# Kernel optimization log

Measured on AMD Instinct MI355X. Metric: run time of the kernel, lower is better.

## Reference

```python
import jax, jax.numpy as jnp
import numpy as np

SEP = 2            # sep_token_id
B, S, H = 8, 4096, 768
MAX_SENT = 64      # = labels.size(1) in the original
STD = 0.02         # initializer_range


def setup_inputs() -> dict:
    key = jax.random.key(0)
    ks = jax.random.split(key, 6)
    hidden = jax.random.normal(ks[0], (B, S, H), jnp.float32)
    ids = jax.random.randint(ks[1], (B, S), 5, 30000, dtype=jnp.int64)
    # plant a sep every 64 tokens -> 64 seps, 64 non-empty sentences per row
    ids = ids.at[:, 63::64].set(SEP)
    W1 = jax.random.normal(ks[2], (H, 4096), jnp.float32) * STD
    b1 = jnp.zeros((4096,), jnp.float32)
    W2 = jax.random.normal(ks[3], (4096, 256), jnp.float32) * STD
    b2 = jnp.zeros((256,), jnp.float32)
    W3 = jax.random.normal(ks[4], (256, 2), jnp.float32) * STD
    b3 = jnp.zeros((2,), jnp.float32)
    return dict(hidden=hidden, input_ids=ids, W1=W1, b1=b1, W2=W2, b2=b2, W3=W3, b3=b3)


def _pool_row(h, ids):
    # h: [S, H], ids: [S] -> per-sentence means [MAX_SENT, H]
    sep = (ids == SEP)
    sep_i = sep.astype(jnp.int32)
    # exclusive cumsum: segment id = number of seps strictly before position t
    seg = jnp.cumsum(sep_i) - sep_i
    pos = jnp.arange(S)
    first_sep = jnp.argmax(sep)
    n_sep = sep_i.sum()
    # original includes the FIRST sep in sentence 0 but excludes later seps,
    # and excludes the last token of the trailing (post-last-sep) segment
    weight = jnp.where(sep, pos == first_sep, True)
    weight = weight & ~((pos == S - 1) & (seg == n_sep) & (n_sep > 0))
    # truncate to max_sentences: overflow segments land in a dump bucket
    seg_c = jnp.minimum(seg, MAX_SENT)
    hw = jnp.where(weight[:, None], h, 0.0)
    sums = jax.ops.segment_sum(hw, seg_c, num_segments=MAX_SENT + 1)[:MAX_SENT]
    cnts = jax.ops.segment_sum(weight.astype(h.dtype), seg_c, num_segments=MAX_SENT + 1)[:MAX_SENT]
    # empty (padding) segments -> zeros, matching the original zero-padding
    return jnp.where(cnts[:, None] > 0, sums / jnp.maximum(cnts, 1.0)[:, None], 0.0)


def reference(hidden, input_ids, W1, b1, W2, b2, W3, b3):
    # [B, MAX_SENT, H] per-sentence mean representations
    sent = jax.vmap(_pool_row)(hidden, input_ids)
    # classifier head (dropout = identity in eval); GELU is exact (torch nn.GELU default)
    x = jax.nn.gelu(jnp.einsum('bmh,hf->bmf', sent, W1) + b1, approximate=False)
    x = jax.nn.gelu(jnp.einsum('bmf,fg->bmg', x, W2) + b2, approximate=False)
    logits = jnp.einsum('bmg,gc->bmc', x, W3) + b3  # [B, MAX_SENT, 2]
    return logits
```

## Files before the change

### kernel.cpp

```cpp
#include <hip/hip_runtime.h>
#include <hip/hip_bf16.h>

#define SEP_ID 2
#define S_LEN  4096
#define HID    768
#define MAXS   64

using short8  = __attribute__((ext_vector_type(8))) short;
using floatx4 = __attribute__((ext_vector_type(4))) float;

__global__ void bounds_kernel(const int* __restrict__ ids,
                              int* __restrict__ sent_start,
                              int* __restrict__ sent_cnt) {
    const int b = blockIdx.x;
    const int t = threadIdx.x;
    const int* row = ids + (size_t)b * S_LEN;

    __shared__ int cnts[256];
    __shared__ int offs[256];
    __shared__ int sep_pos[S_LEN];
    __shared__ int total;

    int local[16];
    int c = 0;
    const int base = t * 16;
    #pragma unroll
    for (int i = 0; i < 16; ++i) {
        if (row[base + i] == SEP_ID) local[c++] = base + i;
    }
    cnts[t] = c;
    __syncthreads();
    if (t == 0) {
        int s = 0;
        for (int i = 0; i < 256; ++i) { offs[i] = s; s += cnts[i]; }
        total = s;
    }
    __syncthreads();
    {
        int o = offs[t];
        for (int i = 0; i < c; ++i) sep_pos[o + i] = local[i];
    }
    __syncthreads();

    const int n_sep = total;
    if (t < MAXS) {
        const int m = t;
        int start = 0, cnt = 0;
        if (n_sep == 0) {
            if (m == 0) { start = 0; cnt = S_LEN; }
        } else if (m < n_sep) {
            if (m == 0) { start = 0; cnt = sep_pos[0] + 1; }
            else { start = sep_pos[m - 1] + 1; cnt = sep_pos[m] - sep_pos[m - 1] - 1; }
        } else if (m == n_sep) {
            start = sep_pos[n_sep - 1] + 1;
            cnt = (S_LEN - 1) - start;
            if (cnt < 0) cnt = 0;
        }
        sent_start[b * MAXS + m] = start;
        sent_cnt[b * MAXS + m]  = cnt;
    }
}

__global__ __launch_bounds__(192) void pool_kernel(const float* __restrict__ hidden,
                                                   const int* __restrict__ sent_start,
                                                   const int* __restrict__ sent_cnt,
                                                   __hip_bfloat16* __restrict__ sent) {
    const int blk = blockIdx.x;
    const int b = blk >> 6;
    const int t = threadIdx.x;
    const int start = sent_start[blk];
    const int cnt   = sent_cnt[blk];

    const float4* base = (const float4*)(hidden + ((size_t)b * S_LEN + start) * HID);
    float ax = 0.f, ay = 0.f, az = 0.f, aw = 0.f;
    int i = 0;
    for (; i + 4 <= cnt; i += 4) {
        float4 v0 = base[(size_t)(i + 0) * 192 + t];
        float4 v1 = base[(size_t)(i + 1) * 192 + t];
        float4 v2 = base[(size_t)(i + 2) * 192 + t];
        float4 v3 = base[(size_t)(i + 3) * 192 + t];
        ax += v0.x + v1.x + v2.x + v3.x;
        ay += v0.y + v1.y + v2.y + v3.y;
        az += v0.z + v1.z + v2.z + v3.z;
        aw += v0.w + v1.w + v2.w + v3.w;
    }
    for (; i < cnt; ++i) {
        float4 v = base[(size_t)i * 192 + t];
        ax += v.x; ay += v.y; az += v.z; aw += v.w;
    }
    const float inv = (cnt > 0) ? 1.0f / (float)cnt : 0.0f;
    __hip_bfloat16* o = sent + (size_t)blk * HID + t * 4;
    o[0] = __float2bfloat16(ax * inv);
    o[1] = __float2bfloat16(ay * inv);
    o[2] = __float2bfloat16(az * inv);
    o[3] = __float2bfloat16(aw * inv);
}

__global__ __launch_bounds__(256) void tconv_kernel(const float* __restrict__ W1,
                                                    const float* __restrict__ W2,
                                                    __hip_bfloat16* __restrict__ W1T,
                                                    __hip_bfloat16* __restrict__ W2T) {
    __shared__ float tile[32][33];
    int id = blockIdx.x;
    const float* in; __hip_bfloat16* out; int K, N, n0, k0;
    if (id < 3072) {
        in = W1; out = W1T; K = 768; N = 4096;
        n0 = (id & 127) * 32; k0 = (id >> 7) * 32;
    } else {
        id -= 3072;
        in = W2; out = W2T; K = 4096; N = 256;
        n0 = (id & 7) * 32; k0 = (id >> 3) * 32;
    }
    const int c = threadIdx.x & 31;
    const int r = threadIdx.x >> 5;
    #pragma unroll
    for (int i = 0; i < 32; i += 8)
        tile[r + i][c] = in[(size_t)(k0 + r + i) * N + n0 + c];
    __syncthreads();
    #pragma unroll
    for (int i = 0; i < 32; i += 8)
        out[(size_t)(n0 + r + i) * K + k0 + c] = __float2bfloat16(tile[c][r + i]);
}

__device__ __forceinline__ float gelu_exact(float x) {
    return 0.5f * x * (1.0f + erff(x * 0.70710678118654752f));
}

__global__ __launch_bounds__(256) void gemm1_kernel(const __hip_bfloat16* __restrict__ A,
                                                    const __hip_bfloat16* __restrict__ BT,
                                                    const float* __restrict__ bias,
                                                    __hip_bfloat16* __restrict__ out) {
    const int n0 = blockIdx.x * 128;
    const int m0 = blockIdx.y * 64;
    const int t = threadIdx.x;
    const int w = t >> 6, l = t & 63;
    const int wm = (w >> 1) * 32;
    const int wn = (w & 1) * 64;

    __shared__ __hip_bfloat16 Al[64][40];
    __shared__ __hip_bfloat16 Bl[128][40];

    floatx4 acc[2][4] = {};

    const int r  = t >> 2;
    const int ch = (t & 3) * 8;
    const __hip_bfloat16* Ag  = A  + (size_t)(m0 + r) * 768 + ch;
    const __hip_bfloat16* Bg0 = BT + (size_t)(n0 + r) * 768 + ch;
    const __hip_bfloat16* Bg1 = BT + (size_t)(n0 + 64 + r) * 768 + ch;

    const int lr = l & 15;
    const int kq = (l >> 4) * 8;

    for (int k0 = 0; k0 < 768; k0 += 32) {
        short8 av  = *(const short8*)(Ag  + k0);
        short8 bv0 = *(const short8*)(Bg0 + k0);
        short8 bv1 = *(const short8*)(Bg1 + k0);
        __syncthreads();
        *(short8*)(&Al[r][ch])      = av;
        *(short8*)(&Bl[r][ch])      = bv0;
        *(short8*)(&Bl[64 + r][ch]) = bv1;
        __syncthreads();

        short8 a0 = *(const short8*)(&Al[wm + lr][kq]);
        short8 a1 = *(const short8*)(&Al[wm + 16 + lr][kq]);
        #pragma unroll
        for (int j = 0; j < 4; ++j) {
            short8 bj = *(const short8*)(&Bl[wn + j * 16 + lr][kq]);
            acc[0][j] = __builtin_amdgcn_mfma_f32_16x16x32_bf16(a0, bj, acc[0][j], 0, 0, 0);
            acc[1][j] = __builtin_amdgcn_mfma_f32_16x16x32_bf16(a1, bj, acc[1][j], 0, 0, 0);
        }
    }

    #pragma unroll
    for (int i = 0; i < 2; ++i) {
        #pragma unroll
        for (int j = 0; j < 4; ++j) {
            const int col  = n0 + wn + j * 16 + lr;
            const int rowb = m0 + wm + i * 16 + (l >> 4) * 4;
            const float bv = bias[col];
            #pragma unroll
            for (int rg = 0; rg < 4; ++rg) {
                float x = acc[i][j][rg] + bv;
                out[(size_t)(rowb + rg) * 4096 + col] = __float2bfloat16(gelu_exact(x));
            }
        }
    }
}

__global__ __launch_bounds__(256) void gemm2_kernel(const __hip_bfloat16* __restrict__ A,
                                                    const __hip_bfloat16* __restrict__ BT,
                                                    float* __restrict__ part) {
    const int n0 = blockIdx.x * 64;
    const int m0 = blockIdx.y * 64;
    const int s  = blockIdx.z;
    const int kb = s * 512;
    const int t = threadIdx.x;
    const int w = t >> 6, l = t & 63;
    const int wm = (w >> 1) * 32;
    const int wn = (w & 1) * 32;

    __shared__ __hip_bfloat16 Al[64][40];
    __shared__ __hip_bfloat16 Bl[64][40];

    floatx4 acc[2][2] = {};

    const int r  = t >> 2;
    const int ch = (t & 3) * 8;
    const __hip_bfloat16* Ag = A  + (size_t)(m0 + r) * 4096 + kb + ch;
    const __hip_bfloat16* Bg = BT + (size_t)(n0 + r) * 4096 + kb + ch;

    const int lr = l & 15;
    const int kq = (l >> 4) * 8;

    for (int k0 = 0; k0 < 512; k0 += 32) {
        short8 av = *(const short8*)(Ag + k0);
        short8 bv = *(const short8*)(Bg + k0);
        __syncthreads();
        *(short8*)(&Al[r][ch]) = av;
        *(short8*)(&Bl[r][ch]) = bv;
        __syncthreads();

        short8 a0 = *(const short8*)(&Al[wm + lr][kq]);
        short8 a1 = *(const short8*)(&Al[wm + 16 + lr][kq]);
        short8 b0 = *(const short8*)(&Bl[wn + lr][kq]);
        short8 b1 = *(const short8*)(&Bl[wn + 16 + lr][kq]);

        acc[0][0] = __builtin_amdgcn_mfma_f32_16x16x32_bf16(a0, b0, acc[0][0], 0, 0, 0);
        acc[0][1] = __builtin_amdgcn_mfma_f32_16x16x32_bf16(a0, b1, acc[0][1], 0, 0, 0);
        acc[1][0] = __builtin_amdgcn_mfma_f32_16x16x32_bf16(a1, b0, acc[1][0], 0, 0, 0);
        acc[1][1] = __builtin_amdgcn_mfma_f32_16x16x32_bf16(a1, b1, acc[1][1], 0, 0, 0);
    }

    float* po = part + (size_t)s * 512 * 256;
    #pragma unroll
    for (int i = 0; i < 2; ++i) {
        #pragma unroll
        for (int j = 0; j < 2; ++j) {
            const int col  = n0 + wn + j * 16 + lr;
            const int rowb = m0 + wm + i * 16 + (l >> 4) * 4;
            #pragma unroll
            for (int rg = 0; rg < 4; ++rg)
                po[(size_t)(rowb + rg) * 256 + col] = acc[i][j][rg];
        }
    }
}

__global__ __launch_bounds__(256) void rh_kernel(const float* __restrict__ part,
                                                 const float* __restrict__ b2,
                                                 const float* __restrict__ W3,
                                                 const float* __restrict__ b3,
                                                 float* __restrict__ out) {
    const int row = blockIdx.x;
    const int c = threadIdx.x;
    const int w = c >> 6, l = c & 63;

    float s = 0.f;
    #pragma unroll
    for (int k = 0; k < 8; ++k)
        s += part[((size_t)k * 512 + row) * 256 + c];
    const float x = gelu_exact(s + b2[c]);
    float y0 = x * W3[c * 2 + 0];
    float y1 = x * W3[c * 2 + 1];
    #pragma unroll
    for (int off = 32; off; off >>= 1) {
        y0 += __shfl_down(y0, off);
        y1 += __shfl_down(y1, off);
    }
    __shared__ float r0[4], r1[4];
    if (l == 0) { r0[w] = y0; r1[w] = y1; }
    __syncthreads();
    if (c == 0) out[row * 2 + 0] = r0[0] + r0[1] + r0[2] + r0[3] + b3[0];
    if (c == 1) out[row * 2 + 1] = r1[0] + r1[1] + r1[2] + r1[3] + b3[1];
}

extern "C" void kernel_launch(void* const* d_in, const int* in_sizes, int n_in,
                              void* d_out, int out_size, void* d_ws, size_t ws_size,
                              hipStream_t stream) {
    const float* hidden = (const float*)d_in[0];
    const int*   ids    = (const int*)d_in[1];
    const float* W1     = (const float*)d_in[2];
    const float* b1     = (const float*)d_in[3];
    const float* W2     = (const float*)d_in[4];
    const float* b2     = (const float*)d_in[5];
    const float* W3     = (const float*)d_in[6];
    const float* b3     = (const float*)d_in[7];
    float* out = (float*)d_out;

    char* ws = (char*)d_ws;
    int* sent_start        = (int*)(ws + 0);
    int* sent_cnt          = (int*)(ws + 2048);
    __hip_bfloat16* sentb  = (__hip_bfloat16*)(ws + 4096);
    __hip_bfloat16* W1T    = (__hip_bfloat16*)(ws + 790528);
    __hip_bfloat16* W2T    = (__hip_bfloat16*)(ws + 7081984);
    __hip_bfloat16* x1     = (__hip_bfloat16*)(ws + 9179136);
    float* part            = (float*)(ws + 13373440);

    bounds_kernel<<<8, 256, 0, stream>>>(ids, sent_start, sent_cnt);
    pool_kernel<<<512, 192, 0, stream>>>(hidden, sent_start, sent_cnt, sentb);
    tconv_kernel<<<4096, 256, 0, stream>>>(W1, W2, W1T, W2T);
    gemm1_kernel<<<dim3(32, 8), 256, 0, stream>>>(sentb, W1T, b1, x1);
    gemm2_kernel<<<dim3(4, 8, 8), 256, 0, stream>>>(x1, W2T, part);
    rh_kernel<<<512, 256, 0, stream>>>(part, b2, W3, b3, out);
}
```

Before: 207.8 us.

## Fuse all stages into one cooperative persistent kernel with grid syncs

```diff
diff --git a/kernel.cpp b/kernel.cpp
--- a/kernel.cpp
+++ b/kernel.cpp
@@ -1,5 +1,8 @@
 #include <hip/hip_runtime.h>
 #include <hip/hip_bf16.h>
+#include <hip/hip_cooperative_groups.h>
+
+namespace cg = cooperative_groups;
 
 #define SEP_ID 2
 #define S_LEN  4096
@@ -9,296 +12,302 @@
 using short8  = __attribute__((ext_vector_type(8))) short;
 using floatx4 = __attribute__((ext_vector_type(4))) float;
 
-__global__ void bounds_kernel(const int* __restrict__ ids,
-                              int* __restrict__ sent_start,
-                              int* __restrict__ sent_cnt) {
-    const int b = blockIdx.x;
-    const int t = threadIdx.x;
-    const int* row = ids + (size_t)b * S_LEN;
-
-    __shared__ int cnts[256];
-    __shared__ int offs[256];
-    __shared__ int sep_pos[S_LEN];
-    __shared__ int total;
-
-    int local[16];
-    int c = 0;
-    const int base = t * 16;
-    #pragma unroll
-    for (int i = 0; i < 16; ++i) {
-        if (row[base + i] == SEP_ID) local[c++] = base + i;
-    }
-    cnts[t] = c;
-    __syncthreads();
-    if (t == 0) {
-        int s = 0;
-        for (int i = 0; i < 256; ++i) { offs[i] = s; s += cnts[i]; }
-        total = s;
-    }
-    __syncthreads();
-    {
-        int o = offs[t];
-        for (int i = 0; i < c; ++i) sep_pos[o + i] = local[i];
-    }
-    __syncthreads();
-
-    const int n_sep = total;
-    if (t < MAXS) {
-        const int m = t;
-        int start = 0, cnt = 0;
-        if (n_sep == 0) {
-            if (m == 0) { start = 0; cnt = S_LEN; }
-        } else if (m < n_sep) {
-            if (m == 0) { start = 0; cnt = sep_pos[0] + 1; }
-            else { start = sep_pos[m - 1] + 1; cnt = sep_pos[m] - sep_pos[m - 1] - 1; }
-        } else if (m == n_sep) {
-            start = sep_pos[n_sep - 1] + 1;
-            cnt = (S_LEN - 1) - start;
-            if (cnt < 0) cnt = 0;
-        }
-        sent_start[b * MAXS + m] = start;
-        sent_cnt[b * MAXS + m]  = cnt;
-    }
-}
-
-__global__ __launch_bounds__(192) void pool_kernel(const float* __restrict__ hidden,
-                                                   const int* __restrict__ sent_start,
-                                                   const int* __restrict__ sent_cnt,
-                                                   __hip_bfloat16* __restrict__ sent) {
-    const int blk = blockIdx.x;
-    const int b = blk >> 6;
-    const int t = threadIdx.x;
-    const int start = sent_start[blk];
-    const int cnt   = sent_cnt[blk];
-
-    const float4* base = (const float4*)(hidden + ((size_t)b * S_LEN + start) * HID);
-    float ax = 0.f, ay = 0.f, az = 0.f, aw = 0.f;
-    int i = 0;
-    for (; i + 4 <= cnt; i += 4) {
-        float4 v0 = base[(size_t)(i + 0) * 192 + t];
-        float4 v1 = base[(size_t)(i + 1) * 192 + t];
-        float4 v2 = base[(size_t)(i + 2) * 192 + t];
-        float4 v3 = base[(size_t)(i + 3) * 192 + t];
-        ax += v0.x + v1.x + v2.x + v3.x;
-        ay += v0.y + v1.y + v2.y + v3.y;
-        az += v0.z + v1.z + v2.z + v3.z;
-        aw += v0.w + v1.w + v2.w + v3.w;
-    }
-    for (; i < cnt; ++i) {
-        float4 v = base[(size_t)i * 192 + t];
-        ax += v.x; ay += v.y; az += v.z; aw += v.w;
-    }
-    const float inv = (cnt > 0) ? 1.0f / (float)cnt : 0.0f;
-    __hip_bfloat16* o = sent + (size_t)blk * HID + t * 4;
-    o[0] = __float2bfloat16(ax * inv);
-    o[1] = __float2bfloat16(ay * inv);
-    o[2] = __float2bfloat16(az * inv);
-    o[3] = __float2bfloat16(aw * inv);
-}
-
-__global__ __launch_bounds__(256) void tconv_kernel(const float* __restrict__ W1,
-                                                    const float* __restrict__ W2,
-                                                    __hip_bfloat16* __restrict__ W1T,
-                                                    __hip_bfloat16* __restrict__ W2T) {
-    __shared__ float tile[32][33];
-    int id = blockIdx.x;
-    const float* in; __hip_bfloat16* out; int K, N, n0, k0;
-    if (id < 3072) {
-        in = W1; out = W1T; K = 768; N = 4096;
-        n0 = (id & 127) * 32; k0 = (id >> 7) * 32;
-    } else {
-        id -= 3072;
-        in = W2; out = W2T; K = 4096; N = 256;
-        n0 = (id & 7) * 32; k0 = (id >> 3) * 32;
-    }
-    const int c = threadIdx.x & 31;
-    const int r = threadIdx.x >> 5;
-    #pragma unroll
-    for (int i = 0; i < 32; i += 8)
-        tile[r + i][c] = in[(size_t)(k0 + r + i) * N + n0 + c];
-    __syncthreads();
-    #pragma unroll
-    for (int i = 0; i < 32; i += 8)
-        out[(size_t)(n0 + r + i) * K + k0 + c] = __float2bfloat16(tile[c][r + i]);
-}
+struct Params {
+    const float* hidden; const int* ids;
+    const float* W1; const float* b1;
+    const float* W2; const float* b2;
+    const float* W3; const float* b3;
+    float* out;
+    int* sent_start; int* sent_cnt;
+    __hip_bfloat16* sentb; __hip_bfloat16* W1T; __hip_bfloat16* W2T;
+    __hip_bfloat16* x1; float* part;
+};
 
 __device__ __forceinline__ float gelu_exact(float x) {
     return 0.5f * x * (1.0f + erff(x * 0.70710678118654752f));
 }
 
-__global__ __launch_bounds__(256) void gemm1_kernel(const __hip_bfloat16* __restrict__ A,
-                                                    const __hip_bfloat16* __restrict__ BT,
-                                                    const float* __restrict__ bias,
-                                                    __hip_bfloat16* __restrict__ out) {
-    const int n0 = blockIdx.x * 128;
-    const int m0 = blockIdx.y * 64;
+__global__ __launch_bounds__(384) void mega_kernel(Params p) {
+    cg::grid_group grid = cg::this_grid();
+    const int blk = blockIdx.x;
     const int t = threadIdx.x;
-    const int w = t >> 6, l = t & 63;
-    const int wm = (w >> 1) * 32;
-    const int wn = (w & 1) * 64;
-
-    __shared__ __hip_bfloat16 Al[64][40];
-    __shared__ __hip_bfloat16 Bl[128][40];
-
-    floatx4 acc[2][4] = {};
-
-    const int r  = t >> 2;
-    const int ch = (t & 3) * 8;
-    const __hip_bfloat16* Ag  = A  + (size_t)(m0 + r) * 768 + ch;
-    const __hip_bfloat16* Bg0 = BT + (size_t)(n0 + r) * 768 + ch;
-    const __hip_bfloat16* Bg1 = BT + (size_t)(n0 + 64 + r) * 768 + ch;
-
-    const int lr = l & 15;
-    const int kq = (l >> 4) * 8;
-
-    for (int k0 = 0; k0 < 768; k0 += 32) {
-        short8 av  = *(const short8*)(Ag  + k0);
-        short8 bv0 = *(const short8*)(Bg0 + k0);
-        short8 bv1 = *(const short8*)(Bg1 + k0);
+
+    __shared__ __align__(16) char smem[18688];
+
+    if (blk < 8) {
+        int* cnts = (int*)smem;
+        int* offs = cnts + 256;
+        int* sep_pos = offs + 256;
+        int* totalp = sep_pos + 4096;
+        const int* row = p.ids + (size_t)blk * S_LEN;
+        int local[16]; int c = 0;
+        if (t < 256) {
+            const int base = t * 16;
+            #pragma unroll
+            for (int i = 0; i < 16; ++i)
+                if (row[base + i] == SEP_ID) local[c++] = base + i;
+            cnts[t] = c;
+        }
         __syncthreads();
-        *(short8*)(&Al[r][ch])      = av;
-        *(short8*)(&Bl[r][ch])      = bv0;
-        *(short8*)(&Bl[64 + r][ch]) = bv1;
+        if (t == 0) {
+            int s = 0;
+            for (int i = 0; i < 256; ++i) { offs[i] = s; s += cnts[i]; }
+            *totalp = s;
+        }
         __syncthreads();
-
-        short8 a0 = *(const short8*)(&Al[wm + lr][kq]);
-        short8 a1 = *(const short8*)(&Al[wm + 16 + lr][kq]);
-        #pragma unroll
-        for (int j = 0; j < 4; ++j) {
-            short8 bj = *(const short8*)(&Bl[wn + j * 16 + lr][kq]);
-            acc[0][j] = __builtin_amdgcn_mfma_f32_16x16x32_bf16(a0, bj, acc[0][j], 0, 0, 0);
-            acc[1][j] = __builtin_amdgcn_mfma_f32_16x16x32_bf16(a1, bj, acc[1][j], 0, 0, 0);
-        }
-    }
-
-    #pragma unroll
-    for (int i = 0; i < 2; ++i) {
-        #pragma unroll
-        for (int j = 0; j < 4; ++j) {
-            const int col  = n0 + wn + j * 16 + lr;
-            const int rowb = m0 + wm + i * 16 + (l >> 4) * 4;
-            const float bv = bias[col];
-            #pragma unroll
-            for (int rg = 0; rg < 4; ++rg) {
-                float x = acc[i][j][rg] + bv;
-                out[(size_t)(rowb + rg) * 4096 + col] = __float2bfloat16(gelu_exact(x));
-            }
-        }
-    }
-}
-
-__global__ __launch_bounds__(256) void gemm2_kernel(const __hip_bfloat16* __restrict__ A,
-                                                    const __hip_bfloat16* __restrict__ BT,
-                                                    float* __restrict__ part) {
-    const int n0 = blockIdx.x * 64;
-    const int m0 = blockIdx.y * 64;
-    const int s  = blockIdx.z;
-    const int kb = s * 512;
-    const int t = threadIdx.x;
-    const int w = t >> 6, l = t & 63;
-    const int wm = (w >> 1) * 32;
-    const int wn = (w & 1) * 32;
-
-    __shared__ __hip_bfloat16 Al[64][40];
-    __shared__ __hip_bfloat16 Bl[64][40];
-
-    floatx4 acc[2][2] = {};
-
-    const int r  = t >> 2;
-    const int ch = (t & 3) * 8;
-    const __hip_bfloat16* Ag = A  + (size_t)(m0 + r) * 4096 + kb + ch;
-    const __hip_bfloat16* Bg = BT + (size_t)(n0 + r) * 4096 + kb + ch;
-
-    const int lr = l & 15;
-    const int kq = (l >> 4) * 8;
-
-    for (int k0 = 0; k0 < 512; k0 += 32) {
-        short8 av = *(const short8*)(Ag + k0);
-        short8 bv = *(const short8*)(Bg + k0);
+        if (t < 256) { int o = offs[t]; for (int i = 0; i < c; ++i) sep_pos[o + i] = local[i]; }
         __syncthreads();
-        *(short8*)(&Al[r][ch]) = av;
-        *(short8*)(&Bl[r][ch]) = bv;
-        __syncthreads();
-
-        short8 a0 = *(const short8*)(&Al[wm + lr][kq]);
-        short8 a1 = *(const short8*)(&Al[wm + 16 + lr][kq]);
-        short8 b0 = *(const short8*)(&Bl[wn + lr][kq]);
-        short8 b1 = *(const short8*)(&Bl[wn + 16 + lr][kq]);
-
-        acc[0][0] = __builtin_amdgcn_mfma_f32_16x16x32_bf16(a0, b0, acc[0][0], 0, 0, 0);
-        acc[0][1] = __builtin_amdgcn_mfma_f32_16x16x32_bf16(a0, b1, acc[0][1], 0, 0, 0);
-        acc[1][0] = __builtin_amdgcn_mfma_f32_16x16x32_bf16(a1, b0, acc[1][0], 0, 0, 0);
-        acc[1][1] = __builtin_amdgcn_mfma_f32_16x16x32_bf16(a1, b1, acc[1][1], 0, 0, 0);
-    }
-
-    float* po = part + (size_t)s * 512 * 256;
-    #pragma unroll
-    for (int i = 0; i < 2; ++i) {
-        #pragma unroll
-        for (int j = 0; j < 2; ++j) {
-            const int col  = n0 + wn + j * 16 + lr;
-            const int rowb = m0 + wm + i * 16 + (l >> 4) * 4;
-            #pragma unroll
-            for (int rg = 0; rg < 4; ++rg)
-                po[(size_t)(rowb + rg) * 256 + col] = acc[i][j][rg];
-        }
-    }
-}
-
-__global__ __launch_bounds__(256) void rh_kernel(const float* __restrict__ part,
-                                                 const float* __restrict__ b2,
-                                                 const float* __restrict__ W3,
-                                                 const float* __restrict__ b3,
-                                                 float* __restrict__ out) {
-    const int row = blockIdx.x;
-    const int c = threadIdx.x;
-    const int w = c >> 6, l = c & 63;
-
-    float s = 0.f;
-    #pragma unroll
-    for (int k = 0; k < 8; ++k)
-        s += part[((size_t)k * 512 + row) * 256 + c];
-    const float x = gelu_exact(s + b2[c]);
-    float y0 = x * W3[c * 2 + 0];
-    float y1 = x * W3[c * 2 + 1];
-    #pragma unroll
-    for (int off = 32; off; off >>= 1) {
-        y0 += __shfl_down(y0, off);
-        y1 += __shfl_down(y1, off);
-    }
-    __shared__ float r0[4], r1[4];
-    if (l == 0) { r0[w] = y0; r1[w] = y1; }
-    __syncthreads();
-    if (c == 0) out[row * 2 + 0] = r0[0] + r0[1] + r0[2] + r0[3] + b3[0];
-    if (c == 1) out[row * 2 + 1] = r1[0] + r1[1] + r1[2] + r1[3] + b3[1];
+        const int n_sep = *totalp;
+        if (t < MAXS) {
+            const int m = t;
+            int start = 0, cnt = 0;
+            if (n_sep == 0) {
+                if (m == 0) { start = 0; cnt = S_LEN; }
+            } else if (m < n_sep) {
+                if (m == 0) { start = 0; cnt = sep_pos[0] + 1; }
+                else { start = sep_pos[m - 1] + 1; cnt = sep_pos[m] - sep_pos[m - 1] - 1; }
+            } else if (m == n_sep) {
+                start = sep_pos[n_sep - 1] + 1;
+                cnt = (S_LEN - 1) - start;
+                if (cnt < 0) cnt = 0;
+            }
+            p.sent_start[blk * MAXS + m] = start;
+            p.sent_cnt[blk * MAXS + m]  = cnt;
+        }
+    } else {
+        float* tile = (float*)smem;
+        const int c = t & 31;
+        const int r = t >> 5;
+        for (int id0 = blk - 8; id0 < 4096; id0 += 248) {
+            const float* in; __hip_bfloat16* outw; int K, N, n0, k0;
+            if (id0 < 3072) { in = p.W1; outw = p.W1T; K = 768;  N = 4096;
+                              n0 = (id0 & 127) * 32; k0 = (id0 >> 7) * 32; }
+            else { const int id = id0 - 3072;
+                   in = p.W2; outw = p.W2T; K = 4096; N = 256;
+                   n0 = (id & 7) * 32; k0 = (id >> 3) * 32; }
+            if (t < 256) {
+                #pragma unroll
+                for (int i = 0; i < 32; i += 8)
+                    tile[(r + i) * 33 + c] = in[(size_t)(k0 + r + i) * N + n0 + c];
+            }
+            __syncthreads();
+            if (t < 256) {
+                #pragma unroll
+                for (int i = 0; i < 32; i += 8)
+                    outw[(size_t)(n0 + r + i) * K + k0 + c] = __float2bfloat16(tile[c * 33 + r + i]);
+            }
+            __syncthreads();
+        }
+    }
+
+    grid.sync();
+
+    {
+        const int which = t / 192;
+        const int u = t - which * 192;
+        const int sidx = blk * 2 + which;
+        const int b = sidx >> 6;
+        const int start = p.sent_start[sidx];
+        const int cnt   = p.sent_cnt[sidx];
+        const float4* base = (const float4*)(p.hidden + ((size_t)b * S_LEN + start) * HID);
+        float ax = 0.f, ay = 0.f, az = 0.f, aw = 0.f;
+        int i = 0;
+        for (; i + 8 <= cnt; i += 8) {
+            float4 v[8];
+            #pragma unroll
+            for (int j = 0; j < 8; ++j) v[j] = base[(size_t)(i + j) * 192 + u];
+            #pragma unroll
+            for (int j = 0; j < 8; ++j) { ax += v[j].x; ay += v[j].y; az += v[j].z; aw += v[j].w; }
+        }
+        for (; i < cnt; ++i) {
+            float4 v = base[(size_t)i * 192 + u];
+            ax += v.x; ay += v.y; az += v.z; aw += v.w;
+        }
+        const float inv = (cnt > 0) ? 1.0f / (float)cnt : 0.0f;
+        __hip_bfloat16* o = p.sentb + (size_t)sidx * HID + u * 4;
+        o[0] = __float2bfloat16(ax * inv);
+        o[1] = __float2bfloat16(ay * inv);
+        o[2] = __float2bfloat16(az * inv);
+        o[3] = __float2bfloat16(aw * inv);
+    }
+
+    grid.sync();
+
+    {
+        const int n0 = (blk & 31) * 128;
+        const int m0 = (blk >> 5) * 64;
+        const int w = t >> 6, l = t & 63;
+        const int wm = (w >> 1) * 32;
+        const int wn = (w & 1) * 64;
+        __hip_bfloat16* Al = (__hip_bfloat16*)smem;
+        __hip_bfloat16* Bl = Al + 64 * 40;
+        floatx4 acc[2][4] = {};
+        const int r  = t >> 2;
+        const int ch = (t & 3) * 8;
+        const __hip_bfloat16 *Ag = nullptr, *Bg0 = nullptr, *Bg1 = nullptr;
+        if (t < 256) {
+            Ag  = p.sentb + (size_t)(m0 + r) * 768 + ch;
+            Bg0 = p.W1T + (size_t)(n0 + r) * 768 + ch;
+            Bg1 = p.W1T + (size_t)(n0 + 64 + r) * 768 + ch;
+        }
+        const int lr = l & 15;
+        const int kq = (l >> 4) * 8;
+        for (int k0 = 0; k0 < 768; k0 += 32) {
+            short8 av, bv0, bv1;
+            if (t < 256) {
+                av  = *(const short8*)(Ag  + k0);
+                bv0 = *(const short8*)(Bg0 + k0);
+                bv1 = *(const short8*)(Bg1 + k0);
+            }
+            __syncthreads();
+            if (t < 256) {
+                *(short8*)(Al + r * 40 + ch)        = av;
+                *(short8*)(Bl + r * 40 + ch)        = bv0;
+                *(short8*)(Bl + (64 + r) * 40 + ch) = bv1;
+            }
+            __syncthreads();
+            if (t < 256) {
+                short8 a0 = *(const short8*)(Al + (wm + lr) * 40 + kq);
+                short8 a1 = *(const short8*)(Al + (wm + 16 + lr) * 40 + kq);
+                #pragma unroll
+                for (int j = 0; j < 4; ++j) {
+                    short8 bj = *(const short8*)(Bl + (wn + j * 16 + lr) * 40 + kq);
+                    acc[0][j] = __builtin_amdgcn_mfma_f32_16x16x32_bf16(a0, bj, acc[0][j], 0, 0, 0);
+                    acc[1][j] = __builtin_amdgcn_mfma_f32_16x16x32_bf16(a1, bj, acc[1][j], 0, 0, 0);
+                }
+            }
+        }
+        if (t < 256) {
+            #pragma unroll
+            for (int i = 0; i < 2; ++i) {
+                #pragma unroll
+                for (int j = 0; j < 4; ++j) {
+                    const int col  = n0 + wn + j * 16 + lr;
+                    const int rowb = m0 + wm + i * 16 + (l >> 4) * 4;
+                    const float bv = p.b1[col];
+                    #pragma unroll
+                    for (int rg = 0; rg < 4; ++rg) {
+                        float x = acc[i][j][rg] + bv;
+                        p.x1[(size_t)(rowb + rg) * 4096 + col] = __float2bfloat16(gelu_exact(x));
+                    }
+                }
+            }
+        }
+    }
+
+    grid.sync();
+
+    {
+        const int n0 = (blk & 3) * 64;
+        const int m0 = ((blk >> 2) & 7) * 64;
+        const int s  = blk >> 5;
+        const int kb = s * 512;
+        const int w = t >> 6, l = t & 63;
+        const int wm = (w >> 1) * 32;
+        const int wn = (w & 1) * 32;
+        __hip_bfloat16* Al = (__hip_bfloat16*)smem;
+        __hip_bfloat16* Bl = Al + 64 * 40;
+        floatx4 acc[2][2] = {};
+        const int r  = t >> 2;
+        const int ch = (t & 3) * 8;
+        const __hip_bfloat16 *Ag = nullptr, *Bg = nullptr;
+        if (t < 256) {
+            Ag = p.x1  + (size_t)(m0 + r) * 4096 + kb + ch;
+            Bg = p.W2T + (size_t)(n0 + r) * 4096 + kb + ch;
+        }
+        const int lr = l & 15;
+        const int kq = (l >> 4) * 8;
+        for (int k0 = 0; k0 < 512; k0 += 32) {
+            short8 av, bv;
+            if (t < 256) { av = *(const short8*)(Ag + k0); bv = *(const short8*)(Bg + k0); }
+            __syncthreads();
+            if (t < 256) {
+                *(short8*)(Al + r * 40 + ch) = av;
+                *(short8*)(Bl + r * 40 + ch) = bv;
+            }
+            __syncthreads();
+            if (t < 256) {
+                short8 a0 = *(const short8*)(Al + (wm + lr) * 40 + kq);
+                short8 a1 = *(const short8*)(Al + (wm + 16 + lr) * 40 + kq);
+                short8 b0 = *(const short8*)(Bl + (wn + lr) * 40 + kq);
+                short8 b1 = *(const short8*)(Bl + (wn + 16 + lr) * 40 + kq);
+                acc[0][0] = __builtin_amdgcn_mfma_f32_16x16x32_bf16(a0, b0, acc[0][0], 0, 0, 0);
+                acc[0][1] = __builtin_amdgcn_mfma_f32_16x16x32_bf16(a0, b1, acc[0][1], 0, 0, 0);
+                acc[1][0] = __builtin_amdgcn_mfma_f32_16x16x32_bf16(a1, b0, acc[1][0], 0, 0, 0);
+                acc[1][1] = __builtin_amdgcn_mfma_f32_16x16x32_bf16(a1, b1, acc[1][1], 0, 0, 0);
+            }
+        }
+        if (t < 256) {
+            float* po = p.part + (size_t)s * 512 * 256;
+            #pragma unroll
+            for (int i = 0; i < 2; ++i) {
+                #pragma unroll
+                for (int j = 0; j < 2; ++j) {
+                    const int col  = n0 + wn + j * 16 + lr;
+                    const int rowb = m0 + wm + i * 16 + (l >> 4) * 4;
+                    #pragma unroll
+                    for (int rg = 0; rg < 4; ++rg)
+                        po[(size_t)(rowb + rg) * 256 + col] = acc[i][j][rg];
+                }
+            }
+        }
+    }
+
+    grid.sync();
+
+    {
+        float* r0 = (float*)smem;
+        float* r1 = r0 + 4;
+        for (int rr = 0; rr < 2; ++rr) {
+            const int row = blk * 2 + rr;
+            float y0 = 0.f, y1 = 0.f;
+            if (t < 256) {
+                float s = 0.f;
+                #pragma unroll
+                for (int k = 0; k < 8; ++k)
+                    s += p.part[((size_t)k * 512 + row) * 256 + t];
+                const float x = gelu_exact(s + p.b2[t]);
+                y0 = x * p.W3[t * 2 + 0];
+                y1 = x * p.W3[t * 2 + 1];
+                #pragma unroll
+                for (int off = 32; off; off >>= 1) {
+                    y0 += __shfl_down(y0, off);
+                    y1 += __shfl_down(y1, off);
+                }
+            }
+            __syncthreads();
+            if (t < 256 && (t & 63) == 0) { r0[t >> 6] = y0; r1[t >> 6] = y1; }
+            __syncthreads();
+            if (t == 0) p.out[row * 2 + 0] = r0[0] + r0[1] + r0[2] + r0[3] + p.b3[0];
+            if (t == 1) p.out[row * 2 + 1] = r1[0] + r1[1] + r1[2] + r1[3] + p.b3[1];
+            __syncthreads();
+        }
+    }
 }
 
 extern "C" void kernel_launch(void* const* d_in, const int* in_sizes, int n_in,
                               void* d_out, int out_size, void* d_ws, size_t ws_size,
                               hipStream_t stream) {
-    const float* hidden = (const float*)d_in[0];
-    const int*   ids    = (const int*)d_in[1];
-    const float* W1     = (const float*)d_in[2];
-    const float* b1     = (const float*)d_in[3];
-    const float* W2     = (const float*)d_in[4];
-    const float* b2     = (const float*)d_in[5];
-    const float* W3     = (const float*)d_in[6];
-    const float* b3     = (const float*)d_in[7];
-    float* out = (float*)d_out;
-
     char* ws = (char*)d_ws;
-    int* sent_start        = (int*)(ws + 0);
-    int* sent_cnt          = (int*)(ws + 2048);
-    __hip_bfloat16* sentb  = (__hip_bfloat16*)(ws + 4096);
-    __hip_bfloat16* W1T    = (__hip_bfloat16*)(ws + 790528);
-    __hip_bfloat16* W2T    = (__hip_bfloat16*)(ws + 7081984);
-    __hip_bfloat16* x1     = (__hip_bfloat16*)(ws + 9179136);
-    float* part            = (float*)(ws + 13373440);
-
-    bounds_kernel<<<8, 256, 0, stream>>>(ids, sent_start, sent_cnt);
-    pool_kernel<<<512, 192, 0, stream>>>(hidden, sent_start, sent_cnt, sentb);
-    tconv_kernel<<<4096, 256, 0, stream>>>(W1, W2, W1T, W2T);
-    gemm1_kernel<<<dim3(32, 8), 256, 0, stream>>>(sentb, W1T, b1, x1);
-    gemm2_kernel<<<dim3(4, 8, 8), 256, 0, stream>>>(x1, W2T, part);
-    rh_kernel<<<512, 256, 0, stream>>>(part, b2, W3, b3, out);
+    Params prm;
+    prm.hidden = (const float*)d_in[0];
+    prm.ids    = (const int*)d_in[1];
+    prm.W1     = (const float*)d_in[2];
+    prm.b1     = (const float*)d_in[3];
+    prm.W2     = (const float*)d_in[4];
+    prm.b2     = (const float*)d_in[5];
+    prm.W3     = (const float*)d_in[6];
+    prm.b3     = (const float*)d_in[7];
+    prm.out    = (float*)d_out;
+    prm.sent_start = (int*)(ws + 0);
+    prm.sent_cnt   = (int*)(ws + 2048);
+    prm.sentb      = (__hip_bfloat16*)(ws + 4096);
+    prm.W1T        = (__hip_bfloat16*)(ws + 790528);
+    prm.W2T        = (__hip_bfloat16*)(ws + 7081984);
+    prm.x1         = (__hip_bfloat16*)(ws + 9179136);
+    prm.part       = (float*)(ws + 13373440);
+
+    void* kargs[] = { (void*)&prm };
+    hipLaunchCooperativeKernel((const void*)mega_kernel, dim3(256), dim3(384),
+                               kargs, 0, stream);
 }
```

New measurement: 354.5 us. 1.71x slower.
